# Kernel tuning notes

Measured on AMD Instinct MI355X. Metric: run time of the kernel, lower is better.

## Reference

```python
import jax, jax.numpy as jnp
import numpy as np

D = 64      # hiddenDims
DQ = 64     # queryDims
M = 64      # inducingPoints
B = 64      # number of ragged segments
LMAX = 4096 # max segment length
Z = float(np.sqrt(DQ))
EPS = 1e-5


def _segment_lengths():
    rng = np.random.default_rng(0)
    return rng.integers(512, LMAX + 1, size=B)


def setup_inputs() -> dict:
    xl = _segment_lengths()
    total = int(xl.sum())
    key = jax.random.key(0)
    ks = jax.random.split(key, 12)
    s = 0.05
    inp = {
        "x": jax.random.normal(ks[0], (total, D), jnp.float32),
        "xlens": jnp.asarray(xl, jnp.int32),
        "I": jax.random.uniform(ks[1], (M, D), jnp.float32),
        # AttentionBlock 0 (queries = inducing points)
        "WQ0": jax.random.normal(ks[2], (DQ, D), jnp.float32) * s,
        "WK0": jax.random.normal(ks[3], (DQ, D), jnp.float32) * s,
        "WV0": jax.random.normal(ks[4], (D, D), jnp.float32) * s,
        "FCw0": jax.random.normal(ks[5], (D, D), jnp.float32) * s,
        "FCb0": jnp.zeros((D,), jnp.float32),
        "g00": jnp.ones((D,), jnp.float32), "b00": jnp.zeros((D,), jnp.float32),
        "g01": jnp.ones((D,), jnp.float32), "b01": jnp.zeros((D,), jnp.float32),
        # AttentionBlock 1 (queries = tokens)
        "WQ1": jax.random.normal(ks[6], (DQ, D), jnp.float32) * s,
        "WK1": jax.random.normal(ks[7], (DQ, D), jnp.float32) * s,
        "WV1": jax.random.normal(ks[8], (D, D), jnp.float32) * s,
        "FCw1": jax.random.normal(ks[9], (D, D), jnp.float32) * s,
        "FCb1": jnp.zeros((D,), jnp.float32),
        "g10": jnp.ones((D,), jnp.float32), "b10": jnp.zeros((D,), jnp.float32),
        "g11": jnp.ones((D,), jnp.float32), "b11": jnp.zeros((D,), jnp.float32),
    }
    return inp


def _ln(x, g, b):
    m = jnp.mean(x, axis=-1, keepdims=True)
    v = jnp.mean(jnp.square(x - m), axis=-1, keepdims=True)
    return (x - m) * jax.lax.rsqrt(v + EPS) * g + b


def _attn_block(q, h, mask_kv, WQ, WK, WV, FCw, FCb, g0, b0, g1, b1):
    # q: [B,Lq,D], h: [B,Lk,D], mask_kv: [B,Lk] or None
    qq = q @ WQ.T                     # [B,Lq,DQ]
    k = h @ WK.T                      # [B,Lk,DQ]
    v = h @ WV.T                      # [B,Lk,D]
    s = jnp.einsum('bqe,bke->bqk', qq, k) / Z
    if mask_kv is not None:
        s = jnp.where(mask_kv[:, None, :], s, -1e30)
    a = jax.nn.softmax(s, axis=-1)
    hh = _ln(q + jnp.einsum('bqk,bkd->bqd', a, v), g0, b0)
    return _ln(hh + jax.nn.relu(hh @ FCw.T + FCb), g1, b1)


def reference(x, xlens, I,
              WQ0, WK0, WV0, FCw0, FCb0, g00, b00, g01, b01,
              WQ1, WK1, WV1, FCw1, FCb1, g10, b10, g11, b11):
    xl = np.asarray(xlens)
    b_idx = np.concatenate([np.full(int(l), b, np.int32) for b, l in enumerate(xl)])
    pos = np.concatenate([np.arange(int(l), dtype=np.int32) for l in xl])
    mask = jnp.asarray(np.arange(LMAX)[None, :] < xl[:, None])   # [B,LMAX]

    padded = jnp.zeros((B, LMAX, D), x.dtype).at[b_idx, pos].set(x)

    # ab0: queries = inducing points (shared), keys/values = set elements
    q0 = jnp.broadcast_to(I[None], (B, M, D))
    i_seg = _attn_block(q0, padded, mask, WQ0, WK0, WV0, FCw0, FCb0, g00, b00, g01, b01)  # [B,M,D]

    # ab1: queries = set elements, keys/values = induced points
    out = _attn_block(padded, i_seg, None, WQ1, WK1, WV1, FCw1, FCb1, g10, b10, g11, b11)  # [B,LMAX,D]

    return out[b_idx, pos]  # flat ragged output [total, D]
```

## Files before the change

kernel.cpp:

```cpp
#include <hip/hip_runtime.h>

#define NB 64
#define NCHUNK 8
#define ZINV 0.125f
#define EPS 1e-5f

typedef __attribute__((ext_vector_type(8))) short short8;
typedef __attribute__((ext_vector_type(4))) float f32x4;
typedef unsigned short ushort_t;

__device__ __forceinline__ f32x4 mm(short8 a, short8 b, f32x4 c) {
  return __builtin_amdgcn_mfma_f32_16x16x32_bf16(a, b, c, 0, 0, 0);
}
__device__ __forceinline__ ushort_t f2bf(float f) {
  unsigned u = __float_as_uint(f);
  u += 0x7fffu + ((u >> 16) & 1u);
  return (ushort_t)(u >> 16);
}
__device__ __forceinline__ unsigned pack2(float a, float b) {
  return (unsigned)f2bf(a) | ((unsigned)f2bf(b) << 16);
}
__device__ __forceinline__ short8 cvt8(float4 a, float4 b) {
  union { unsigned u[4]; short8 s; } z;
  z.u[0] = pack2(a.x, a.y); z.u[1] = pack2(a.z, a.w);
  z.u[2] = pack2(b.x, b.y); z.u[3] = pack2(b.z, b.w);
  return z.s;
}
__device__ __forceinline__ void cvt16(const float* __restrict__ src, ushort_t* dst) {
  const float4* s = (const float4*)src;
  unsigned* d = (unsigned*)dst;
  float4 A0 = s[0], A1 = s[1], A2 = s[2], A3 = s[3];
  d[0] = pack2(A0.x, A0.y); d[1] = pack2(A0.z, A0.w);
  d[2] = pack2(A1.x, A1.y); d[3] = pack2(A1.z, A1.w);
  d[4] = pack2(A2.x, A2.y); d[5] = pack2(A2.z, A2.w);
  d[6] = pack2(A3.x, A3.y); d[7] = pack2(A3.z, A3.w);
}

__global__ __launch_bounds__(256) void k_setup(const int* __restrict__ xlens,
                                               const float* __restrict__ I,
                                               const float* __restrict__ WQ0,
                                               const float* __restrict__ WK0,
                                               const float* __restrict__ FCw1,
                                               const float* __restrict__ WV0,
                                               const float* __restrict__ FCw0,
                                               const float* __restrict__ WK1,
                                               const float* __restrict__ WQ1,
                                               const float* __restrict__ WV1,
                                               int* __restrict__ off,
                                               ushort_t* __restrict__ QK0bf,
                                               ushort_t* __restrict__ Wfcbf,
                                               ushort_t* __restrict__ WV0bf,
                                               ushort_t* __restrict__ FCw0bf,
                                               ushort_t* __restrict__ WK1bf,
                                               ushort_t* __restrict__ WQ1Tbf,
                                               ushort_t* __restrict__ WV1bf) {
  int tid = threadIdx.x;
  if (tid < 64) {
    int v = xlens[tid];
#pragma unroll
    for (int d = 1; d < 64; d <<= 1) {
      int t = __shfl_up(v, d);
      if (tid >= d) v += t;
    }
    off[tid + 1] = v;
    if (tid == 0) off[0] = 0;
  }
  __shared__ ushort_t Ibf[64][72];
  __shared__ ushort_t Wq0[64][72];
  __shared__ ushort_t Wk0T[64][72];
  __shared__ ushort_t qqbf[64][72];

  int w = tid >> 6, l = tid & 63, l15 = l & 15, lh = l >> 4;
  int srow = tid >> 2, sc0 = (tid & 3) << 4;
  int so = srow * 64 + sc0;

  cvt16(I + so, &Ibf[srow][sc0]);
  cvt16(WQ0 + so, &Wq0[srow][sc0]);
  {
    const float* s = WK0 + so;
#pragma unroll
    for (int i = 0; i < 16; ++i) Wk0T[sc0 + i][srow] = f2bf(s[i]);
  }
  cvt16(FCw1 + so, Wfcbf + so);
  cvt16(WV0 + so, WV0bf + so);
  cvt16(FCw0 + so, FCw0bf + so);
  cvt16(WK1 + so, WK1bf + so);
  cvt16(WV1 + so, WV1bf + so);
  {
    const float* s = WQ1 + so;
#pragma unroll
    for (int i = 0; i < 16; ++i) WQ1Tbf[(sc0 + i) * 64 + srow] = f2bf(s[i]);
  }
  __syncthreads();

  short8 ai0 = *(const short8*)&Ibf[16 * w + l15][lh * 8];
  short8 ai1 = *(const short8*)&Ibf[16 * w + l15][32 + lh * 8];
  f32x4 cA[4];
#pragma unroll
  for (int n = 0; n < 4; ++n) {
    short8 b0 = *(const short8*)&Wq0[16 * n + l15][lh * 8];
    short8 b1 = *(const short8*)&Wq0[16 * n + l15][32 + lh * 8];
    cA[n] = mm(ai0, b0, (f32x4){0.f, 0.f, 0.f, 0.f});
    cA[n] = mm(ai1, b1, cA[n]);
  }
#pragma unroll
  for (int n = 0; n < 4; ++n)
#pragma unroll
    for (int r = 0; r < 4; ++r)
      qqbf[16 * w + 4 * lh + r][16 * n + l15] = f2bf(cA[n][r]);

  short8 aq0 = *(const short8*)&qqbf[16 * w + l15][lh * 8];
  short8 aq1 = *(const short8*)&qqbf[16 * w + l15][32 + lh * 8];
  f32x4 cB[4];
#pragma unroll
  for (int n = 0; n < 4; ++n) {
    short8 b0 = *(const short8*)&Wk0T[16 * n + l15][lh * 8];
    short8 b1 = *(const short8*)&Wk0T[16 * n + l15][32 + lh * 8];
    cB[n] = mm(aq0, b0, (f32x4){0.f, 0.f, 0.f, 0.f});
    cB[n] = mm(aq1, b1, cB[n]);
  }
#pragma unroll
  for (int n = 0; n < 4; ++n)
#pragma unroll
    for (int r = 0; r < 4; ++r)
      QK0bf[(16 * w + 4 * lh + r) * 64 + 16 * n + l15] = f2bf(cB[n][r] * ZINV);
}

__global__ __launch_bounds__(256) void k_phaseA(const float* __restrict__ x,
                                                const int* __restrict__ off,
                                                const ushort_t* __restrict__ QK0bf,
                                                float* __restrict__ part_mx,
                                                float* __restrict__ part_sm,
                                                float* __restrict__ part_ax) {
  int b = blockIdx.x / NCHUNK, chunk = blockIdx.x % NCHUNK;
  int s0 = off[b], L = off[b + 1] - s0;
  int clen = (L + NCHUNK - 1) / NCHUNK;
  int t0 = chunk * clen;
  int t1 = t0 + clen; if (t1 > L) t1 = L;

  __shared__ ushort_t xbf[64][72];
  __shared__ ushort_t xT[64][72];
  __shared__ ushort_t pbf[64][72];

  int tid = threadIdx.x;
  int w = tid >> 6, l = tid & 63, l15 = l & 15, lh = l >> 4;
  int srow = tid >> 2, sc0 = (tid & 3) << 4;

  short8 aq0 = *(const short8*)(QK0bf + ((16 * w + l15) << 6) + lh * 8);
  short8 aq1 = *(const short8*)(QK0bf + ((16 * w + l15) << 6) + 32 + lh * 8);

  float mx[4], sm[4];
#pragma unroll
  for (int r = 0; r < 4; ++r) { mx[r] = -1e30f; sm[r] = 0.f; }
  f32x4 acc[4];
#pragma unroll
  for (int n = 0; n < 4; ++n) acc[n] = (f32x4){0.f, 0.f, 0.f, 0.f};

  float4 P0, P1, P2, P3;
  {
    int g = t0 + srow;
    int gc = g < t1 ? g : t1 - 1;
    const float4* src = (const float4*)(x + ((size_t)(s0 + gc) << 6) + sc0);
    P0 = src[0]; P1 = src[1]; P2 = src[2]; P3 = src[3];
  }

  for (int tt = t0; tt < t1; tt += 64) {
    __syncthreads();
    {
      float vv[16] = {P0.x, P0.y, P0.z, P0.w, P1.x, P1.y, P1.z, P1.w,
                      P2.x, P2.y, P2.z, P2.w, P3.x, P3.y, P3.z, P3.w};
      unsigned* dst = (unsigned*)&xbf[srow][sc0];
      dst[0] = pack2(vv[0], vv[1]);   dst[1] = pack2(vv[2], vv[3]);
      dst[2] = pack2(vv[4], vv[5]);   dst[3] = pack2(vv[6], vv[7]);
      dst[4] = pack2(vv[8], vv[9]);   dst[5] = pack2(vv[10], vv[11]);
      dst[6] = pack2(vv[12], vv[13]); dst[7] = pack2(vv[14], vv[15]);
#pragma unroll
      for (int i = 0; i < 16; ++i) xT[sc0 + i][srow] = f2bf(vv[i]);
    }
    __syncthreads();
    if (tt + 64 < t1) {
      int g = tt + 64 + srow;
      int gc = g < t1 ? g : t1 - 1;
      const float4* src = (const float4*)(x + ((size_t)(s0 + gc) << 6) + sc0);
      P0 = src[0]; P1 = src[1]; P2 = src[2]; P3 = src[3];
    }
    f32x4 c1[4];
#pragma unroll
    for (int n = 0; n < 4; ++n) {
      short8 bx0 = *(const short8*)&xbf[16 * n + l15][lh * 8];
      short8 bx1 = *(const short8*)&xbf[16 * n + l15][32 + lh * 8];
      c1[n] = mm(aq0, bx0, (f32x4){0.f, 0.f, 0.f, 0.f});
      c1[n] = mm(aq1, bx1, c1[n]);
    }
    bool val[4];
#pragma unroll
    for (int n = 0; n < 4; ++n) val[n] = (tt + 16 * n + l15) < t1;

    float p[4][4];
#pragma unroll
    for (int r = 0; r < 4; ++r) {
      float tmax = -1e30f;
#pragma unroll
      for (int n = 0; n < 4; ++n) tmax = fmaxf(tmax, val[n] ? c1[n][r] : -1e30f);
      tmax = fmaxf(tmax, __shfl_xor(tmax, 1));
      tmax = fmaxf(tmax, __shfl_xor(tmax, 2));
      tmax = fmaxf(tmax, __shfl_xor(tmax, 4));
      tmax = fmaxf(tmax, __shfl_xor(tmax, 8));
      float nm = fmaxf(mx[r], tmax);
      float f = __expf(mx[r] - nm);
      mx[r] = nm;
      float psum = 0.f;
#pragma unroll
      for (int n = 0; n < 4; ++n) {
        float pv = val[n] ? __expf(c1[n][r] - nm) : 0.f;
        p[n][r] = pv;
        psum += pv;
      }
      psum += __shfl_xor(psum, 1);
      psum += __shfl_xor(psum, 2);
      psum += __shfl_xor(psum, 4);
      psum += __shfl_xor(psum, 8);
      sm[r] = sm[r] * f + psum;
#pragma unroll
      for (int n = 0; n < 4; ++n) acc[n][r] *= f;
    }
#pragma unroll
    for (int n = 0; n < 4; ++n)
#pragma unroll
      for (int r = 0; r < 4; ++r)
        pbf[16 * w + 4 * lh + r][16 * n + l15] = f2bf(p[n][r]);
    short8 pa0 = *(const short8*)&pbf[16 * w + l15][lh * 8];
    short8 pa1 = *(const short8*)&pbf[16 * w + l15][32 + lh * 8];
#pragma unroll
    for (int n = 0; n < 4; ++n) {
      short8 bt0 = *(const short8*)&xT[16 * n + l15][lh * 8];
      short8 bt1 = *(const short8*)&xT[16 * n + l15][32 + lh * 8];
      acc[n] = mm(pa0, bt0, acc[n]);
      acc[n] = mm(pa1, bt1, acc[n]);
    }
  }
  int base = (b * NCHUNK + chunk) * 64;
  if (l15 == 0) {
#pragma unroll
    for (int r = 0; r < 4; ++r) {
      int m = 16 * w + 4 * lh + r;
      part_mx[base + m] = mx[r];
      part_sm[base + m] = sm[r];
    }
  }
#pragma unroll
  for (int n = 0; n < 4; ++n)
#pragma unroll
    for (int r = 0; r < 4; ++r) {
      int m = 16 * w + 4 * lh + r;
      part_ax[((size_t)(base + m) << 6) + 16 * n + l15] = acc[n][r];
    }
}

__global__ __launch_bounds__(256) void k_combine(const float* __restrict__ part_mx,
                                                 const float* __restrict__ part_sm,
                                                 const float* __restrict__ part_ax,
                                                 const float* __restrict__ I,
                                                 const ushort_t* __restrict__ WV0bf,
                                                 const ushort_t* __restrict__ FCw0bf,
                                                 const float* __restrict__ FCb0,
                                                 const float* __restrict__ g00,
                                                 const float* __restrict__ b00,
                                                 const float* __restrict__ g01,
                                                 const float* __restrict__ b01,
                                                 const ushort_t* __restrict__ WK1bf,
                                                 const ushort_t* __restrict__ WQ1Tbf,
                                                 const ushort_t* __restrict__ WV1bf,
                                                 ushort_t* __restrict__ K1fbf,
                                                 ushort_t* __restrict__ V1Tbf) {
  int b = blockIdx.x;
  int tid = threadIdx.x;
  int w = tid >> 6, l = tid & 63, l15 = l & 15, lh = l >> 4;

  __shared__ ushort_t av[64][72];
  __shared__ ushort_t sb[64][72];

  {
    int m = tid >> 2, dq = tid & 3, e0 = dq << 4;
    float Mx = -1e30f;
#pragma unroll
    for (int c = 0; c < NCHUNK; ++c)
      Mx = fmaxf(Mx, part_mx[(b * NCHUNK + c) * 64 + m]);
    float S = 0.f;
    float ax[16];
#pragma unroll
    for (int i = 0; i < 16; ++i) ax[i] = 0.f;
#pragma unroll
    for (int c = 0; c < NCHUNK; ++c) {
      int pb = (b * NCHUNK + c) * 64 + m;
      float f = __expf(part_mx[pb] - Mx);
      S += part_sm[pb] * f;
      const f32x4* pa = (const f32x4*)(part_ax + ((size_t)pb << 6) + e0);
#pragma unroll
      for (int qd = 0; qd < 4; ++qd) {
        f32x4 v = pa[qd];
#pragma unroll
        for (int j = 0; j < 4; ++j) ax[qd * 4 + j] += v[j] * f;
      }
    }
    float invS = 1.f / S;
    unsigned* dst = (unsigned*)&av[m][e0];
#pragma unroll
    for (int i = 0; i < 8; ++i)
      dst[i] = pack2(ax[2 * i] * invS, ax[2 * i + 1] * invS);
  }
  __syncthreads();

  float p00[4], q00[4], p01[4], q01[4], fcb[4];
#pragma unroll
  for (int n = 0; n < 4; ++n) {
    int d = 16 * n + l15;
    p00[n] = g00[d]; q00[n] = b00[d];
    p01[n] = g01[d]; q01[n] = b01[d];
    fcb[n] = FCb0[d];
  }
  int row = 16 * w + 4 * lh;

  short8 a0 = *(const short8*)&av[16 * w + l15][lh * 8];
  short8 a1 = *(const short8*)&av[16 * w + l15][32 + lh * 8];
  f32x4 c1[4];
#pragma unroll
  for (int n = 0; n < 4; ++n) {
    short8 b0 = *(const short8*)(WV0bf + ((16 * n + l15) << 6) + lh * 8);
    short8 b1 = *(const short8*)(WV0bf + ((16 * n + l15) << 6) + 32 + lh * 8);
    c1[n] = mm(a0, b0, (f32x4){0.f, 0.f, 0.f, 0.f});
    c1[n] = mm(a1, b1, c1[n]);
  }
  float hh[4][4];
#pragma unroll
  for (int r = 0; r < 4; ++r) {
    float h[4];
#pragma unroll
    for (int n = 0; n < 4; ++n)
      h[n] = c1[n][r] + I[(row + r) * 64 + 16 * n + l15];
    float s1 = h[0] + h[1] + h[2] + h[3];
    s1 += __shfl_xor(s1, 1); s1 += __shfl_xor(s1, 2);
    s1 += __shfl_xor(s1, 4); s1 += __shfl_xor(s1, 8);
    float mean = s1 * 0.015625f;
    float s2 = 0.f;
#pragma unroll
    for (int n = 0; n < 4; ++n) { float c = h[n] - mean; s2 += c * c; }
    s2 += __shfl_xor(s2, 1); s2 += __shfl_xor(s2, 2);
    s2 += __shfl_xor(s2, 4); s2 += __shfl_xor(s2, 8);
    float rs = rsqrtf(s2 * 0.015625f + EPS);
#pragma unroll
    for (int n = 0; n < 4; ++n) {
      hh[n][r] = (h[n] - mean) * rs * p00[n] + q00[n];
      sb[row + r][16 * n + l15] = f2bf(hh[n][r]);
    }
  }
  short8 h0 = *(const short8*)&sb[16 * w + l15][lh * 8];
  short8 h1 = *(const short8*)&sb[16 * w + l15][32 + lh * 8];
  f32x4 c2[4];
#pragma unroll
  for (int n = 0; n < 4; ++n) {
    short8 b0 = *(const short8*)(FCw0bf + ((16 * n + l15) << 6) + lh * 8);
    short8 b1 = *(const short8*)(FCw0bf + ((16 * n + l15) << 6) + 32 + lh * 8);
    c2[n] = mm(h0, b0, (f32x4){0.f, 0.f, 0.f, 0.f});
    c2[n] = mm(h1, b1, c2[n]);
  }
#pragma unroll
  for (int r = 0; r < 4; ++r) {
    float u[4];
#pragma unroll
    for (int n = 0; n < 4; ++n)
      u[n] = hh[n][r] + fmaxf(c2[n][r] + fcb[n], 0.f);
    float s1 = u[0] + u[1] + u[2] + u[3];
    s1 += __shfl_xor(s1, 1); s1 += __shfl_xor(s1, 2);
    s1 += __shfl_xor(s1, 4); s1 += __shfl_xor(s1, 8);
    float mean = s1 * 0.015625f;
    float s2 = 0.f;
#pragma unroll
    for (int n = 0; n < 4; ++n) { float c = u[n] - mean; s2 += c * c; }
    s2 += __shfl_xor(s2, 1); s2 += __shfl_xor(s2, 2);
    s2 += __shfl_xor(s2, 4); s2 += __shfl_xor(s2, 8);
    float rs = rsqrtf(s2 * 0.015625f + EPS);
#pragma unroll
    for (int n = 0; n < 4; ++n)
      av[row + r][16 * n + l15] = f2bf((u[n] - mean) * rs * p01[n] + q01[n]);
  }
  short8 i0 = *(const short8*)&av[16 * w + l15][lh * 8];
  short8 i1 = *(const short8*)&av[16 * w + l15][32 + lh * 8];
  f32x4 c3[4];
#pragma unroll
  for (int n = 0; n < 4; ++n) {
    short8 b0 = *(const short8*)(WK1bf + ((16 * n + l15) << 6) + lh * 8);
    short8 b1 = *(const short8*)(WK1bf + ((16 * n + l15) << 6) + 32 + lh * 8);
    c3[n] = mm(i0, b0, (f32x4){0.f, 0.f, 0.f, 0.f});
    c3[n] = mm(i1, b1, c3[n]);
  }
#pragma unroll
  for (int n = 0; n < 4; ++n)
#pragma unroll
    for (int r = 0; r < 4; ++r)
      sb[row + r][16 * n + l15] = f2bf(c3[n][r]);
  short8 t0f = *(const short8*)&sb[16 * w + l15][lh * 8];
  short8 t1f = *(const short8*)&sb[16 * w + l15][32 + lh * 8];
  f32x4 c4[4];
#pragma unroll
  for (int n = 0; n < 4; ++n) {
    short8 b0 = *(const short8*)(WQ1Tbf + ((16 * n + l15) << 6) + lh * 8);
    short8 b1 = *(const short8*)(WQ1Tbf + ((16 * n + l15) << 6) + 32 + lh * 8);
    c4[n] = mm(t0f, b0, (f32x4){0.f, 0.f, 0.f, 0.f});
    c4[n] = mm(t1f, b1, c4[n]);
  }
#pragma unroll
  for (int n = 0; n < 4; ++n)
#pragma unroll
    for (int r = 0; r < 4; ++r)
      K1fbf[((size_t)(b * 64 + row + r) << 6) + 16 * n + l15] = f2bf(c4[n][r] * ZINV);
  f32x4 c5[4];
#pragma unroll
  for (int n = 0; n < 4; ++n) {
    short8 b0 = *(const short8*)(WV1bf + ((16 * n + l15) << 6) + lh * 8);
    short8 b1 = *(const short8*)(WV1bf + ((16 * n + l15) << 6) + 32 + lh * 8);
    c5[n] = mm(i0, b0, (f32x4){0.f, 0.f, 0.f, 0.f});
    c5[n] = mm(i1, b1, c5[n]);
  }
#pragma unroll
  for (int n = 0; n < 4; ++n)
#pragma unroll
    for (int r = 0; r < 4; ++r)
      V1Tbf[((size_t)(b * 64 + 16 * n + l15) << 6) + row + r] = f2bf(c5[n][r]);
}

__global__ __launch_bounds__(256) void k_phaseB(const float* __restrict__ x,
                                                const int* __restrict__ off,
                                                const ushort_t* __restrict__ K1fbf,
                                                const ushort_t* __restrict__ V1Tbf,
                                                const ushort_t* __restrict__ Wfcbf,
                                                const float* __restrict__ FCb1,
                                                const float* __restrict__ g10,
                                                const float* __restrict__ b10,
                                                const float* __restrict__ g11,
                                                const float* __restrict__ b11,
                                                float* __restrict__ outp) {
  int b = blockIdx.x >> 6, tile = blockIdx.x & 63;
  int s0 = off[b], L = off[b + 1] - s0;
  int t0 = tile << 6;
  if (t0 >= L) return;
  int nt = L - t0; if (nt > 64) nt = 64;

  __shared__ ushort_t pbf[64][72];

  int tid = threadIdx.x;
  int w = tid >> 6, l = tid & 63, l15 = l & 15, lh = l >> 4;

  int rA = 16 * w + l15;
  if (rA >= nt) rA = nt - 1;
  const float* xr = x + ((size_t)(s0 + t0 + rA) << 6);
  float4 xa0 = *(const float4*)(xr + lh * 8);
  float4 xa1 = *(const float4*)(xr + lh * 8 + 4);
  float4 xa2 = *(const float4*)(xr + 32 + lh * 8);
  float4 xa3 = *(const float4*)(xr + 32 + lh * 8 + 4);
  float res[4][4];
#pragma unroll
  for (int r = 0; r < 4; ++r) {
    int rr = 16 * w + 4 * lh + r;
    if (rr >= nt) rr = nt - 1;
    const float* rp = x + ((size_t)(s0 + t0 + rr) << 6);
#pragma unroll
    for (int n = 0; n < 4; ++n) res[n][r] = rp[16 * n + l15];
  }
  float gg0[4], bb0[4], gg1[4], bb1[4], fb[4];
#pragma unroll
  for (int n = 0; n < 4; ++n) {
    int d = 16 * n + l15;
    gg0[n] = g10[d]; bb0[n] = b10[d];
    gg1[n] = g11[d]; bb1[n] = b11[d];
    fb[n] = FCb1[d];
  }
  short8 a0 = cvt8(xa0, xa1);
  short8 a1 = cvt8(xa2, xa3);
  const ushort_t* Kb = K1fbf + ((size_t)b << 12);
  f32x4 c1[4];
#pragma unroll
  for (int n = 0; n < 4; ++n) {
    short8 bk0 = *(const short8*)(Kb + ((16 * n + l15) << 6) + lh * 8);
    short8 bk1 = *(const short8*)(Kb + ((16 * n + l15) << 6) + 32 + lh * 8);
    c1[n] = mm(a0, bk0, (f32x4){0.f, 0.f, 0.f, 0.f});
    c1[n] = mm(a1, bk1, c1[n]);
  }
  float inv[4];
#pragma unroll
  for (int r = 0; r < 4; ++r) {
    float mxr = fmaxf(fmaxf(c1[0][r], c1[1][r]), fmaxf(c1[2][r], c1[3][r]));
    mxr = fmaxf(mxr, __shfl_xor(mxr, 1));
    mxr = fmaxf(mxr, __shfl_xor(mxr, 2));
    mxr = fmaxf(mxr, __shfl_xor(mxr, 4));
    mxr = fmaxf(mxr, __shfl_xor(mxr, 8));
    float s = 0.f;
#pragma unroll
    for (int n = 0; n < 4; ++n) {
      float p = __expf(c1[n][r] - mxr);
      c1[n][r] = p;
      s += p;
    }
    s += __shfl_xor(s, 1);
    s += __shfl_xor(s, 2);
    s += __shfl_xor(s, 4);
    s += __shfl_xor(s, 8);
    inv[r] = 1.f / s;
  }
#pragma unroll
  for (int n = 0; n < 4; ++n)
#pragma unroll
    for (int r = 0; r < 4; ++r)
      pbf[16 * w + 4 * lh + r][16 * n + l15] = f2bf(c1[n][r]);
  short8 pa0 = *(const short8*)&pbf[16 * w + l15][lh * 8];
  short8 pa1 = *(const short8*)&pbf[16 * w + l15][32 + lh * 8];
  const ushort_t* Vb = V1Tbf + ((size_t)b << 12);
  f32x4 c2[4];
#pragma unroll
  for (int n = 0; n < 4; ++n) {
    short8 bv0 = *(const short8*)(Vb + ((16 * n + l15) << 6) + lh * 8);
    short8 bv1 = *(const short8*)(Vb + ((16 * n + l15) << 6) + 32 + lh * 8);
    c2[n] = mm(pa0, bv0, (f32x4){0.f, 0.f, 0.f, 0.f});
    c2[n] = mm(pa1, bv1, c2[n]);
  }
  float hh[4][4];
#pragma unroll
  for (int r = 0; r < 4; ++r) {
    int t = 16 * w + 4 * lh + r;
    float h[4];
#pragma unroll
    for (int n = 0; n < 4; ++n)
      h[n] = c2[n][r] * inv[r] + res[n][r];
    float s1 = h[0] + h[1] + h[2] + h[3];
    s1 += __shfl_xor(s1, 1); s1 += __shfl_xor(s1, 2);
    s1 += __shfl_xor(s1, 4); s1 += __shfl_xor(s1, 8);
    float mean = s1 * 0.015625f;
    float s2 = 0.f;
#pragma unroll
    for (int n = 0; n < 4; ++n) { float c = h[n] - mean; s2 += c * c; }
    s2 += __shfl_xor(s2, 1); s2 += __shfl_xor(s2, 2);
    s2 += __shfl_xor(s2, 4); s2 += __shfl_xor(s2, 8);
    float rs = rsqrtf(s2 * 0.015625f + EPS);
#pragma unroll
    for (int n = 0; n < 4; ++n) {
      hh[n][r] = (h[n] - mean) * rs * gg0[n] + bb0[n];
      pbf[t][16 * n + l15] = f2bf(hh[n][r]);
    }
  }
  short8 ha0 = *(const short8*)&pbf[16 * w + l15][lh * 8];
  short8 ha1 = *(const short8*)&pbf[16 * w + l15][32 + lh * 8];
  f32x4 c3[4];
#pragma unroll
  for (int n = 0; n < 4; ++n) {
    short8 bw0 = *(const short8*)(Wfcbf + ((16 * n + l15) << 6) + lh * 8);
    short8 bw1 = *(const short8*)(Wfcbf + ((16 * n + l15) << 6) + 32 + lh * 8);
    c3[n] = mm(ha0, bw0, (f32x4){0.f, 0.f, 0.f, 0.f});
    c3[n] = mm(ha1, bw1, c3[n]);
  }
#pragma unroll
  for (int r = 0; r < 4; ++r) {
    int t = 16 * w + 4 * lh + r;
    float u[4];
#pragma unroll
    for (int n = 0; n < 4; ++n)
      u[n] = hh[n][r] + fmaxf(c3[n][r] + fb[n], 0.f);
    float s1 = u[0] + u[1] + u[2] + u[3];
    s1 += __shfl_xor(s1, 1); s1 += __shfl_xor(s1, 2);
    s1 += __shfl_xor(s1, 4); s1 += __shfl_xor(s1, 8);
    float mean = s1 * 0.015625f;
    float s2 = 0.f;
#pragma unroll
    for (int n = 0; n < 4; ++n) { float c = u[n] - mean; s2 += c * c; }
    s2 += __shfl_xor(s2, 1); s2 += __shfl_xor(s2, 2);
    s2 += __shfl_xor(s2, 4); s2 += __shfl_xor(s2, 8);
    float rs = rsqrtf(s2 * 0.015625f + EPS);
    if (t < nt) {
#pragma unroll
      for (int n = 0; n < 4; ++n)
        outp[((size_t)(s0 + t0 + t) << 6) + 16 * n + l15] =
            (u[n] - mean) * rs * gg1[n] + bb1[n];
    }
  }
}


extern "C" void kernel_launch(void* const* d_in, const int* in_sizes, int n_in,
                              void* d_out, int out_size, void* d_ws, size_t ws_size,
                              hipStream_t stream) {
  const float* x    = (const float*)d_in[0];
  const int*   xlen = (const int*)d_in[1];
  const float* I    = (const float*)d_in[2];
  const float* WQ0  = (const float*)d_in[3];
  const float* WK0  = (const float*)d_in[4];
  const float* WV0  = (const float*)d_in[5];
  const float* FCw0 = (const float*)d_in[6];
  const float* FCb0 = (const float*)d_in[7];
  const float* g00  = (const float*)d_in[8];
  const float* b00  = (const float*)d_in[9];
  const float* g01  = (const float*)d_in[10];
  const float* b01  = (const float*)d_in[11];
  const float* WQ1  = (const float*)d_in[12];
  const float* WK1  = (const float*)d_in[13];
  const float* WV1  = (const float*)d_in[14];
  const float* FCw1 = (const float*)d_in[15];
  const float* FCb1 = (const float*)d_in[16];
  const float* g10  = (const float*)d_in[17];
  const float* b10  = (const float*)d_in[18];
  const float* g11  = (const float*)d_in[19];
  const float* b11  = (const float*)d_in[20];

  char* p = (char*)d_ws;
  int* off = (int*)p;                p += 1024;
  ushort_t* QK0bf = (ushort_t*)p;    p += 64 * 64 * 2;
  ushort_t* Wfcbf = (ushort_t*)p;    p += 64 * 64 * 2;
  ushort_t* WV0bf = (ushort_t*)p;    p += 64 * 64 * 2;
  ushort_t* FCw0bf = (ushort_t*)p;   p += 64 * 64 * 2;
  ushort_t* WK1bf = (ushort_t*)p;    p += 64 * 64 * 2;
  ushort_t* WQ1Tbf = (ushort_t*)p;   p += 64 * 64 * 2;
  ushort_t* WV1bf = (ushort_t*)p;    p += 64 * 64 * 2;
  ushort_t* K1fbf = (ushort_t*)p;    p += (size_t)NB * 64 * 64 * 2;
  ushort_t* V1Tbf = (ushort_t*)p;    p += (size_t)NB * 64 * 64 * 2;
  float* pmx = (float*)p;            p += (size_t)NB * NCHUNK * 64 * 4;
  float* psm = (float*)p;            p += (size_t)NB * NCHUNK * 64 * 4;
  float* pax = (float*)p;

  k_setup<<<1, 256, 0, stream>>>(xlen, I, WQ0, WK0, FCw1, WV0, FCw0, WK1, WQ1, WV1,
                                 off, QK0bf, Wfcbf, WV0bf, FCw0bf, WK1bf, WQ1Tbf, WV1bf);
  k_phaseA<<<NB * NCHUNK, 256, 0, stream>>>(x, off, QK0bf, pmx, psm, pax);
  k_combine<<<NB, 256, 0, stream>>>(pmx, psm, pax, I, WV0bf, FCw0bf, FCb0,
                                    g00, b00, g01, b01, WK1bf, WQ1Tbf, WV1bf,
                                    K1fbf, V1Tbf);
  k_phaseB<<<NB * 64, 256, 0, stream>>>(x, off, K1fbf, V1Tbf, Wfcbf, FCb1,
                                        g10, b10, g11, b11, (float*)d_out);
}
```

Measured before the change: 93.89 us.

## Make phaseB blocks loop over strided tiles with next-tile prefetch of x

Launches NB*16 blocks instead of NB*64. Each block walks its segment's 64-token tiles with a stride of 16 and register-prefetches the next tile's x rows while computing the current one. This cuts the many early-exit blocks, amortises the per-block parameter loads, and overlaps global loads with MFMA and softmax work. In exchange there is less parallelism for latency hiding, more register pressure, and possible load imbalance across segments of different lengths.

```diff
diff --git a/kernel.cpp b/kernel.cpp
--- a/kernel.cpp
+++ b/kernel.cpp
@@ -2,6 +2,7 @@
 
 #define NB 64
 #define NCHUNK 8
+#define NSUB 16
 #define ZINV 0.125f
 #define EPS 1e-5f
 
@@ -440,33 +441,16 @@
                                                 const float* __restrict__ g11,
                                                 const float* __restrict__ b11,
                                                 float* __restrict__ outp) {
-  int b = blockIdx.x >> 6, tile = blockIdx.x & 63;
+  int b = blockIdx.x / NSUB, sub = blockIdx.x % NSUB;
   int s0 = off[b], L = off[b + 1] - s0;
-  int t0 = tile << 6;
-  if (t0 >= L) return;
-  int nt = L - t0; if (nt > 64) nt = 64;
+  int tiles = (L + 63) >> 6;
+  if (sub >= tiles) return;
 
   __shared__ ushort_t pbf[64][72];
 
   int tid = threadIdx.x;
   int w = tid >> 6, l = tid & 63, l15 = l & 15, lh = l >> 4;
 
-  int rA = 16 * w + l15;
-  if (rA >= nt) rA = nt - 1;
-  const float* xr = x + ((size_t)(s0 + t0 + rA) << 6);
-  float4 xa0 = *(const float4*)(xr + lh * 8);
-  float4 xa1 = *(const float4*)(xr + lh * 8 + 4);
-  float4 xa2 = *(const float4*)(xr + 32 + lh * 8);
-  float4 xa3 = *(const float4*)(xr + 32 + lh * 8 + 4);
-  float res[4][4];
-#pragma unroll
-  for (int r = 0; r < 4; ++r) {
-    int rr = 16 * w + 4 * lh + r;
-    if (rr >= nt) rr = nt - 1;
-    const float* rp = x + ((size_t)(s0 + t0 + rr) << 6);
-#pragma unroll
-    for (int n = 0; n < 4; ++n) res[n][r] = rp[16 * n + l15];
-  }
   float gg0[4], bb0[4], gg1[4], bb1[4], fb[4];
 #pragma unroll
   for (int n = 0; n < 4; ++n) {
@@ -475,111 +459,151 @@
     gg1[n] = g11[d]; bb1[n] = b11[d];
     fb[n] = FCb1[d];
   }
-  short8 a0 = cvt8(xa0, xa1);
-  short8 a1 = cvt8(xa2, xa3);
   const ushort_t* Kb = K1fbf + ((size_t)b << 12);
-  f32x4 c1[4];
-#pragma unroll
-  for (int n = 0; n < 4; ++n) {
-    short8 bk0 = *(const short8*)(Kb + ((16 * n + l15) << 6) + lh * 8);
-    short8 bk1 = *(const short8*)(Kb + ((16 * n + l15) << 6) + 32 + lh * 8);
-    c1[n] = mm(a0, bk0, (f32x4){0.f, 0.f, 0.f, 0.f});
-    c1[n] = mm(a1, bk1, c1[n]);
-  }
-  float inv[4];
-#pragma unroll
-  for (int r = 0; r < 4; ++r) {
-    float mxr = fmaxf(fmaxf(c1[0][r], c1[1][r]), fmaxf(c1[2][r], c1[3][r]));
-    mxr = fmaxf(mxr, __shfl_xor(mxr, 1));
-    mxr = fmaxf(mxr, __shfl_xor(mxr, 2));
-    mxr = fmaxf(mxr, __shfl_xor(mxr, 4));
-    mxr = fmaxf(mxr, __shfl_xor(mxr, 8));
-    float s = 0.f;
+  const ushort_t* Vb = V1Tbf + ((size_t)b << 12);
+
+  float4 xa0, xa1, xa2, xa3;
+  {
+    int t0 = sub << 6;
+    int nt = L - t0; if (nt > 64) nt = 64;
+    int rA = 16 * w + l15; if (rA >= nt) rA = nt - 1;
+    const float* xr = x + ((size_t)(s0 + t0 + rA) << 6);
+    xa0 = *(const float4*)(xr + lh * 8);
+    xa1 = *(const float4*)(xr + lh * 8 + 4);
+    xa2 = *(const float4*)(xr + 32 + lh * 8);
+    xa3 = *(const float4*)(xr + 32 + lh * 8 + 4);
+  }
+
+  for (int j = sub; j < tiles; j += NSUB) {
+    int t0 = j << 6;
+    int nt = L - t0; if (nt > 64) nt = 64;
+
+    float4 xn0 = xa0, xn1 = xa1, xn2 = xa2, xn3 = xa3;
+    int jn = j + NSUB;
+    if (jn < tiles) {
+      int t0n = jn << 6;
+      int ntn = L - t0n; if (ntn > 64) ntn = 64;
+      int rAn = 16 * w + l15; if (rAn >= ntn) rAn = ntn - 1;
+      const float* xrn = x + ((size_t)(s0 + t0n + rAn) << 6);
+      xn0 = *(const float4*)(xrn + lh * 8);
+      xn1 = *(const float4*)(xrn + lh * 8 + 4);
+      xn2 = *(const float4*)(xrn + 32 + lh * 8);
+      xn3 = *(const float4*)(xrn + 32 + lh * 8 + 4);
+    }
+    float res[4][4];
+#pragma unroll
+    for (int r = 0; r < 4; ++r) {
+      int rr = 16 * w + 4 * lh + r;
+      if (rr >= nt) rr = nt - 1;
+      const float* rp = x + ((size_t)(s0 + t0 + rr) << 6);
+#pragma unroll
+      for (int n = 0; n < 4; ++n) res[n][r] = rp[16 * n + l15];
+    }
+    short8 a0 = cvt8(xa0, xa1);
+    short8 a1 = cvt8(xa2, xa3);
+    f32x4 c1[4];
 #pragma unroll
     for (int n = 0; n < 4; ++n) {
-      float p = __expf(c1[n][r] - mxr);
-      c1[n][r] = p;
-      s += p;
-    }
-    s += __shfl_xor(s, 1);
-    s += __shfl_xor(s, 2);
-    s += __shfl_xor(s, 4);
-    s += __shfl_xor(s, 8);
-    inv[r] = 1.f / s;
-  }
-#pragma unroll
-  for (int n = 0; n < 4; ++n)
-#pragma unroll
-    for (int r = 0; r < 4; ++r)
-      pbf[16 * w + 4 * lh + r][16 * n + l15] = f2bf(c1[n][r]);
-  short8 pa0 = *(const short8*)&pbf[16 * w + l15][lh * 8];
-  short8 pa1 = *(const short8*)&pbf[16 * w + l15][32 + lh * 8];
-  const ushort_t* Vb = V1Tbf + ((size_t)b << 12);
-  f32x4 c2[4];
-#pragma unroll
-  for (int n = 0; n < 4; ++n) {
-    short8 bv0 = *(const short8*)(Vb + ((16 * n + l15) << 6) + lh * 8);
-    short8 bv1 = *(const short8*)(Vb + ((16 * n + l15) << 6) + 32 + lh * 8);
-    c2[n] = mm(pa0, bv0, (f32x4){0.f, 0.f, 0.f, 0.f});
-    c2[n] = mm(pa1, bv1, c2[n]);
-  }
-  float hh[4][4];
-#pragma unroll
-  for (int r = 0; r < 4; ++r) {
-    int t = 16 * w + 4 * lh + r;
-    float h[4];
+      short8 bk0 = *(const short8*)(Kb + ((16 * n + l15) << 6) + lh * 8);
+      short8 bk1 = *(const short8*)(Kb + ((16 * n + l15) << 6) + 32 + lh * 8);
+      c1[n] = mm(a0, bk0, (f32x4){0.f, 0.f, 0.f, 0.f});
+      c1[n] = mm(a1, bk1, c1[n]);
+    }
+    float inv[4];
+#pragma unroll
+    for (int r = 0; r < 4; ++r) {
+      float mxr = fmaxf(fmaxf(c1[0][r], c1[1][r]), fmaxf(c1[2][r], c1[3][r]));
+      mxr = fmaxf(mxr, __shfl_xor(mxr, 1));
+      mxr = fmaxf(mxr, __shfl_xor(mxr, 2));
+      mxr = fmaxf(mxr, __shfl_xor(mxr, 4));
+      mxr = fmaxf(mxr, __shfl_xor(mxr, 8));
+      float s = 0.f;
+#pragma unroll
+      for (int n = 0; n < 4; ++n) {
+        float p = __expf(c1[n][r] - mxr);
+        c1[n][r] = p;
+        s += p;
+      }
+      s += __shfl_xor(s, 1);
+      s += __shfl_xor(s, 2);
+      s += __shfl_xor(s, 4);
+      s += __shfl_xor(s, 8);
+      inv[r] = 1.f / s;
+    }
 #pragma unroll
     for (int n = 0; n < 4; ++n)
-      h[n] = c2[n][r] * inv[r] + res[n][r];
-    float s1 = h[0] + h[1] + h[2] + h[3];
-    s1 += __shfl_xor(s1, 1); s1 += __shfl_xor(s1, 2);
-    s1 += __shfl_xor(s1, 4); s1 += __shfl_xor(s1, 8);
-    float mean = s1 * 0.015625f;
-    float s2 = 0.f;
-#pragma unroll
-    for (int n = 0; n < 4; ++n) { float c = h[n] - mean; s2 += c * c; }
-    s2 += __shfl_xor(s2, 1); s2 += __shfl_xor(s2, 2);
-    s2 += __shfl_xor(s2, 4); s2 += __shfl_xor(s2, 8);
-    float rs = rsqrtf(s2 * 0.015625f + EPS);
+#pragma unroll
+      for (int r = 0; r < 4; ++r)
+        pbf[16 * w + 4 * lh + r][16 * n + l15] = f2bf(c1[n][r]);
+    short8 pa0 = *(const short8*)&pbf[16 * w + l15][lh * 8];
+    short8 pa1 = *(const short8*)&pbf[16 * w + l15][32 + lh * 8];
+    f32x4 c2[4];
 #pragma unroll
     for (int n = 0; n < 4; ++n) {
-      hh[n][r] = (h[n] - mean) * rs * gg0[n] + bb0[n];
-      pbf[t][16 * n + l15] = f2bf(hh[n][r]);
-    }
-  }
-  short8 ha0 = *(const short8*)&pbf[16 * w + l15][lh * 8];
-  short8 ha1 = *(const short8*)&pbf[16 * w + l15][32 + lh * 8];
-  f32x4 c3[4];
-#pragma unroll
-  for (int n = 0; n < 4; ++n) {
-    short8 bw0 = *(const short8*)(Wfcbf + ((16 * n + l15) << 6) + lh * 8);
-    short8 bw1 = *(const short8*)(Wfcbf + ((16 * n + l15) << 6) + 32 + lh * 8);
-    c3[n] = mm(ha0, bw0, (f32x4){0.f, 0.f, 0.f, 0.f});
-    c3[n] = mm(ha1, bw1, c3[n]);
-  }
-#pragma unroll
-  for (int r = 0; r < 4; ++r) {
-    int t = 16 * w + 4 * lh + r;
-    float u[4];
-#pragma unroll
-    for (int n = 0; n < 4; ++n)
-      u[n] = hh[n][r] + fmaxf(c3[n][r] + fb[n], 0.f);
-    float s1 = u[0] + u[1] + u[2] + u[3];
-    s1 += __shfl_xor(s1, 1); s1 += __shfl_xor(s1, 2);
-    s1 += __shfl_xor(s1, 4); s1 += __shfl_xor(s1, 8);
-    float mean = s1 * 0.015625f;
-    float s2 = 0.f;
-#pragma unroll
-    for (int n = 0; n < 4; ++n) { float c = u[n] - mean; s2 += c * c; }
-    s2 += __shfl_xor(s2, 1); s2 += __shfl_xor(s2, 2);
-    s2 += __shfl_xor(s2, 4); s2 += __shfl_xor(s2, 8);
-    float rs = rsqrtf(s2 * 0.015625f + EPS);
-    if (t < nt) {
+      short8 bv0 = *(const short8*)(Vb + ((16 * n + l15) << 6) + lh * 8);
+      short8 bv1 = *(const short8*)(Vb + ((16 * n + l15) << 6) + 32 + lh * 8);
+      c2[n] = mm(pa0, bv0, (f32x4){0.f, 0.f, 0.f, 0.f});
+      c2[n] = mm(pa1, bv1, c2[n]);
+    }
+    float hh[4][4];
+#pragma unroll
+    for (int r = 0; r < 4; ++r) {
+      int t = 16 * w + 4 * lh + r;
+      float h[4];
 #pragma unroll
       for (int n = 0; n < 4; ++n)
-        outp[((size_t)(s0 + t0 + t) << 6) + 16 * n + l15] =
-            (u[n] - mean) * rs * gg1[n] + bb1[n];
-    }
+        h[n] = c2[n][r] * inv[r] + res[n][r];
+      float s1 = h[0] + h[1] + h[2] + h[3];
+      s1 += __shfl_xor(s1, 1); s1 += __shfl_xor(s1, 2);
+      s1 += __shfl_xor(s1, 4); s1 += __shfl_xor(s1, 8);
+      float mean = s1 * 0.015625f;
+      float s2 = 0.f;
+#pragma unroll
+      for (int n = 0; n < 4; ++n) { float c = h[n] - mean; s2 += c * c; }
+      s2 += __shfl_xor(s2, 1); s2 += __shfl_xor(s2, 2);
+      s2 += __shfl_xor(s2, 4); s2 += __shfl_xor(s2, 8);
+      float rs = rsqrtf(s2 * 0.015625f + EPS);
+#pragma unroll
+      for (int n = 0; n < 4; ++n) {
+        hh[n][r] = (h[n] - mean) * rs * gg0[n] + bb0[n];
+        pbf[t][16 * n + l15] = f2bf(hh[n][r]);
+      }
+    }
+    short8 ha0 = *(const short8*)&pbf[16 * w + l15][lh * 8];
+    short8 ha1 = *(const short8*)&pbf[16 * w + l15][32 + lh * 8];
+    f32x4 c3[4];
+#pragma unroll
+    for (int n = 0; n < 4; ++n) {
+      short8 bw0 = *(const short8*)(Wfcbf + ((16 * n + l15) << 6) + lh * 8);
+      short8 bw1 = *(const short8*)(Wfcbf + ((16 * n + l15) << 6) + 32 + lh * 8);
+      c3[n] = mm(ha0, bw0, (f32x4){0.f, 0.f, 0.f, 0.f});
+      c3[n] = mm(ha1, bw1, c3[n]);
+    }
+#pragma unroll
+    for (int r = 0; r < 4; ++r) {
+      int t = 16 * w + 4 * lh + r;
+      float u[4];
+#pragma unroll
+      for (int n = 0; n < 4; ++n)
+        u[n] = hh[n][r] + fmaxf(c3[n][r] + fb[n], 0.f);
+      float s1 = u[0] + u[1] + u[2] + u[3];
+      s1 += __shfl_xor(s1, 1); s1 += __shfl_xor(s1, 2);
+      s1 += __shfl_xor(s1, 4); s1 += __shfl_xor(s1, 8);
+      float mean = s1 * 0.015625f;
+      float s2 = 0.f;
+#pragma unroll
+      for (int n = 0; n < 4; ++n) { float c = u[n] - mean; s2 += c * c; }
+      s2 += __shfl_xor(s2, 1); s2 += __shfl_xor(s2, 2);
+      s2 += __shfl_xor(s2, 4); s2 += __shfl_xor(s2, 8);
+      float rs = rsqrtf(s2 * 0.015625f + EPS);
+      if (t < nt) {
+#pragma unroll
+        for (int n = 0; n < 4; ++n)
+          outp[((size_t)(s0 + t0 + t) << 6) + 16 * n + l15] =
+              (u[n] - mean) * rs * gg1[n] + bb1[n];
+      }
+    }
+    xa0 = xn0; xa1 = xn1; xa2 = xn2; xa3 = xn3;
   }
 }
 
@@ -630,6 +654,6 @@
   k_combine<<<NB, 256, 0, stream>>>(pmx, psm, pax, I, WV0bf, FCw0bf, FCb0,
                                     g00, b00, g01, b01, WK1bf, WQ1Tbf, WV1bf,
                                     K1fbf, V1Tbf);
-  k_phaseB<<<NB * 64, 256, 0, stream>>>(x, off, K1fbf, V1Tbf, Wfcbf, FCb1,
-                                        g10, b10, g11, b11, (float*)d_out);
-}
+  k_phaseB<<<NB * NSUB, 256, 0, stream>>>(x, off, K1fbf, V1Tbf, Wfcbf, FCb1,
+                                          g10, b10, g11, b11, (float*)d_out);
+}
```

Result: faster. 90.10 us (-4.0%).
